# Optimization experiments

Measured on AMD Instinct MI355X. Metric: run time of the kernel, lower is better.

## Reference

```python
import jax, jax.numpy as jnp
import numpy as np

GAMMA = 5e-4
IN_DIM, HID = 512, 4096
N = HID  # batch must equal hidden_dim for classifier(gram) to type-check


def setup_inputs() -> dict:
    key = jax.random.key(0)
    ks = jax.random.split(key, 7)
    s = lambda fan_in: 1.0 / np.sqrt(fan_in)
    return {
        "x": jax.random.normal(ks[0], (N, IN_DIM), jnp.float32),
        "W1": jax.random.uniform(ks[1], (HID, IN_DIM), jnp.float32, -s(IN_DIM), s(IN_DIM)),
        "b1": jax.random.uniform(ks[2], (HID,), jnp.float32, -s(IN_DIM), s(IN_DIM)),
        "W2": jax.random.uniform(ks[3], (HID, HID), jnp.float32, -s(HID), s(HID)),
        "b2": jax.random.uniform(ks[4], (HID,), jnp.float32, -s(HID), s(HID)),
        "Wc": jax.random.uniform(ks[5], (1, HID), jnp.float32, -s(HID), s(HID)),
        "bc": jax.random.uniform(ks[6], (1,), jnp.float32, -s(HID), s(HID)),
    }


def reference(x, W1, b1, W2, b2, Wc, bc):
    h = jnp.tanh(x @ W1.T + b1)          # [N, HID]
    h = jnp.tanh(h @ W2.T + b2)          # [N, HID]
    # KernelLayer: support = h.detach() (first call), RBF gram via cdist+exp
    support = jax.lax.stop_gradient(h)   # [N, HID]
    sq = (jnp.sum(h * h, axis=1, keepdims=True)
          + jnp.sum(support * support, axis=1)[None, :]
          - 2.0 * (h @ support.T))       # [N, N] squared distances
    gram = jnp.exp(-GAMMA * sq)
    return gram @ Wc.T + bc              # [N, 1]
```

## Files before the change

### kernel.cpp

```cpp
#include <hip/hip_runtime.h>
#include <hip/hip_bf16.h>


#define NROWS 4096
#define HID   4096
#define INDIM 512
#define GAMMA_F 5e-4f

typedef float f32x4  __attribute__((ext_vector_type(4)));
typedef int   i32x4  __attribute__((ext_vector_type(4)));
typedef int   i32x8  __attribute__((ext_vector_type(8)));

#define SCALE1 0x7F7F7F7F

#define MFMA16(d, a, b) \
    d = __builtin_amdgcn_mfma_scale_f32_16x16x128_f8f6f4( \
        a, b, d, 0, 0, 0, SCALE1, 0, SCALE1)

__device__ __forceinline__ unsigned char f2e4m3(float x) {
  unsigned int u = __float_as_uint(x);
  unsigned char s = (unsigned char)((u >> 24) & 0x80u);
  float a = fabsf(x);
  if (a >= 448.f) return s | 0x7E;
  if (a < 0.015625f) {
    int q = (int)rintf(a * 512.f);
    return s | (unsigned char)q;
  }
  unsigned int ua = u & 0x7fffffffu;
  ua += 0x7FFFFu + ((ua >> 20) & 1u);
  int e = (int)(ua >> 23) - 127;
  unsigned int m = (ua >> 20) & 7u;
  return s | (unsigned char)(((e + 7) << 3) | m);
}

__global__ void prep(const float* __restrict__ x, const float* __restrict__ W1,
                     const float* __restrict__ W2, const float* __restrict__ bc,
                     unsigned char* __restrict__ xq, unsigned char* __restrict__ w1q,
                     unsigned char* __restrict__ w2q,
                     float* __restrict__ out, float* __restrict__ norms) {
  const int gi = blockIdx.x * blockDim.x + threadIdx.x;
  if (gi < NROWS) { out[gi] = bc[0]; norms[gi] = 0.f; }
  const int NX  = NROWS * INDIM / 8;
  const int NW2 = HID * HID / 8;
  const int total = 2 * NX + NW2;
  const int stride = gridDim.x * blockDim.x;
  for (int i = gi; i < total; i += stride) {
    const float* src; unsigned char* dst; float sc; int j;
    if (i < NX)          { src = x;  dst = xq;  sc = 16.f;  j = i; }
    else if (i < 2 * NX) { src = W1; dst = w1q; sc = 32.f;  j = i - NX; }
    else                 { src = W2; dst = w2q; sc = 128.f; j = i - 2 * NX; }
    float4 v0 = ((const float4*)src)[j * 2];
    float4 v1 = ((const float4*)src)[j * 2 + 1];
    unsigned int r0 = (unsigned int)f2e4m3(v0.x * sc)
                    | ((unsigned int)f2e4m3(v0.y * sc) << 8)
                    | ((unsigned int)f2e4m3(v0.z * sc) << 16)
                    | ((unsigned int)f2e4m3(v0.w * sc) << 24);
    unsigned int r1 = (unsigned int)f2e4m3(v1.x * sc)
                    | ((unsigned int)f2e4m3(v1.y * sc) << 8)
                    | ((unsigned int)f2e4m3(v1.z * sc) << 16)
                    | ((unsigned int)f2e4m3(v1.w * sc) << 24);
    uint2 o; o.x = r0; o.y = r1;
    ((uint2*)dst)[j] = o;
  }
}

__device__ __forceinline__ void gload16(const void* g, void* l) {
  __builtin_amdgcn_global_load_lds(
      (const __attribute__((address_space(1))) void*)g,
      (__attribute__((address_space(3))) void*)l, 16, 0, 0);
}

#define LDFRAG(dst, base0, off, RSTRIDE) do {                       \
    i32x4 lo_ = *(const i32x4*)((base0) + (off));                   \
    i32x4 hi_ = *(const i32x4*)((base0) + (RSTRIDE) + (off));       \
    dst = __builtin_shufflevector(lo_, hi_, 0, 1, 2, 3, 4, 5, 6, 7); } while (0)

template <int EPI>
__global__ __launch_bounds__(256, 4)
void gemm128_fp8(const unsigned char* __restrict__ A, const unsigned char* __restrict__ B,
                 int K, int N,
                 const float* __restrict__ bias, unsigned char* __restrict__ Hout,
                 float* __restrict__ norms_out) {
  __shared__ __align__(16) unsigned char As[2][128 * 64];
  __shared__ __align__(16) unsigned char Bs[2][128 * 64];

  const int tid  = threadIdx.x;
  const int lane = tid & 63;
  const int wave = tid >> 6;
  const int wr = wave >> 1, wc = wave & 1;
  const int fr = lane & 15, fq = lane >> 4;

  const int nwg = gridDim.x;
  const int cpx = nwg >> 3;
  const int bid = blockIdx.x;
  const int swzb = (bid & 7) * cpx + (bid >> 3);
  const int nbx = N >> 7;
  const int brow = (swzb / nbx) << 7;
  const int bcol = (swzb % nbx) << 7;

  const unsigned char* ap[4]; const unsigned char* bp[4]; int ldq[4];
#pragma unroll
  for (int q = 0; q < 4; ++q) {
    int idx = q * 256 + tid;
    int h   = idx >> 9;
    int row = (idx >> 2) & 127;
    int c   = idx & 3;
    int gcol = ((((c ^ ((row >> 1) & 3)) << 1) | h) << 4);
    ap[q] = A + (size_t)(brow + row) * K + gcol;
    bp[q] = B + (size_t)(bcol + row) * K + gcol;
    ldq[q] = (q * 256 + wave * 64) * 16;
  }

  int aoff[4], boff[4];
#pragma unroll
  for (int mi = 0; mi < 4; ++mi) {
    int row = wr * 64 + mi * 16 + fr;
    aoff[mi] = row * 64 + ((fq ^ ((row >> 1) & 3)) << 4);
  }
#pragma unroll
  for (int nj = 0; nj < 4; ++nj) {
    int row = wc * 64 + nj * 16 + fr;
    boff[nj] = row * 64 + ((fq ^ ((row >> 1) & 3)) << 4);
  }

  f32x4 acc[4][4] = {};

  for (int t = 0; t < (K >> 7); ++t) {
    __syncthreads();
    {
      int kk = t * 128;
      gload16(ap[0] + kk, &As[0][0] + ldq[0]);
      gload16(ap[1] + kk, &As[0][0] + ldq[1]);
      gload16(ap[2] + kk, &As[0][0] + ldq[2]);
      gload16(ap[3] + kk, &As[0][0] + ldq[3]);
      gload16(bp[0] + kk, &Bs[0][0] + ldq[0]);
      gload16(bp[1] + kk, &Bs[0][0] + ldq[1]);
      gload16(bp[2] + kk, &Bs[0][0] + ldq[2]);
      gload16(bp[3] + kk, &Bs[0][0] + ldq[3]);
    }
    __syncthreads();

    i32x8 af[4], bf[4];
#pragma unroll
    for (int mi = 0; mi < 4; ++mi) LDFRAG(af[mi], &As[0][0], aoff[mi], 8192);
#pragma unroll
    for (int nj = 0; nj < 4; ++nj) LDFRAG(bf[nj], &Bs[0][0], boff[nj], 8192);
#pragma unroll
    for (int mi = 0; mi < 4; ++mi)
#pragma unroll
      for (int nj = 0; nj < 4; ++nj) MFMA16(acc[mi][nj], af[mi], bf[nj]);
  }

  const float rescale = (EPI == 0) ? (1.f / 512.f) : (1.f / 1024.f);
  float bv[4];
#pragma unroll
  for (int nj = 0; nj < 4; ++nj) bv[nj] = bias[bcol + wc * 64 + nj * 16 + fr];
#pragma unroll
  for (int mi = 0; mi < 4; ++mi) {
    int row0 = brow + wr * 64 + mi * 16 + fq * 4;
#pragma unroll
    for (int rr = 0; rr < 4; ++rr) {
      float ns = 0.f;
#pragma unroll
      for (int nj = 0; nj < 4; ++nj) {
        int col = bcol + wc * 64 + nj * 16 + fr;
        float v = tanhf(acc[mi][nj][rr] * rescale + bv[nj]);
        Hout[(size_t)(row0 + rr) * N + col] = f2e4m3(8.f * v);
        if (EPI == 2) ns += v * v;
      }
      if (EPI == 2) {
        ns += __shfl_xor(ns, 1);
        ns += __shfl_xor(ns, 2);
        ns += __shfl_xor(ns, 4);
        ns += __shfl_xor(ns, 8);
        if (fr == 0) atomicAdd(&norms_out[row0 + rr], ns);
      }
    }
  }
}

__global__ __launch_bounds__(256, 2)
void gram_tri(const unsigned char* __restrict__ H, int K,
              const float* __restrict__ norms, const float* __restrict__ Wc,
              float* __restrict__ out) {
  __shared__ __align__(16) unsigned char As[2][128 * 64];
  __shared__ __align__(16) unsigned char Bs[2][128 * 64];

  const int tid  = threadIdx.x;
  const int lane = tid & 63;
  const int wave = tid >> 6;
  const int wr = wave >> 1, wc = wave & 1;
  const int fr = lane & 15, fq = lane >> 4;

  const int bid = blockIdx.x;
  const int swzb = (bid & 7) * 66 + (bid >> 3);
  int I = (int)((sqrtf(8.0f * (float)swzb + 1.0f) - 1.0f) * 0.5f);
  while ((I + 1) * (I + 2) / 2 <= swzb) ++I;
  while (I * (I + 1) / 2 > swzb) --I;
  const int J = swzb - I * (I + 1) / 2;
  const int brow = I << 7, bcol = J << 7;
  const bool diag = (I == J);

  const unsigned char* ap[4]; const unsigned char* bp[4]; int wq[4];
#pragma unroll
  for (int q = 0; q < 4; ++q) {
    int idx = q * 256 + tid;
    int h   = idx >> 9;
    int row = (idx >> 2) & 127;
    int c   = idx & 3;
    int gcol = ((((c ^ ((row >> 1) & 3)) << 1) | h) << 4);
    ap[q] = H + (size_t)(brow + row) * K + gcol;
    bp[q] = H + (size_t)(bcol + row) * K + gcol;
    wq[q] = idx * 16;
  }

  int aoff[4], boff[4];
#pragma unroll
  for (int mi = 0; mi < 4; ++mi) {
    int row = wr * 64 + mi * 16 + fr;
    aoff[mi] = row * 64 + ((fq ^ ((row >> 1) & 3)) << 4);
  }
#pragma unroll
  for (int nj = 0; nj < 4; ++nj) {
    int row = wc * 64 + nj * 16 + fr;
    boff[nj] = row * 64 + ((fq ^ ((row >> 1) & 3)) << 4);
  }

  const int NT = K >> 7;
  f32x4 acc[4][4] = {};
  i32x4 rA[4], rB[4];

#pragma unroll
  for (int q = 0; q < 4; ++q) {
    rA[q] = *(const i32x4*)(ap[q]);
    rB[q] = *(const i32x4*)(bp[q]);
  }
#pragma unroll
  for (int q = 0; q < 4; ++q) {
    *(i32x4*)(&As[0][0] + wq[q]) = rA[q];
    *(i32x4*)(&Bs[0][0] + wq[q]) = rB[q];
  }
  __syncthreads();

  for (int t = 0; t < NT; ++t) {
    int tn = t + 1; if (tn >= NT) tn = NT - 1;
#pragma unroll
    for (int q = 0; q < 4; ++q) {
      rA[q] = *(const i32x4*)(ap[q] + tn * 128);
      rB[q] = *(const i32x4*)(bp[q] + tn * 128);
    }

    i32x8 af[4], bf[4];
#pragma unroll
    for (int mi = 0; mi < 4; ++mi) LDFRAG(af[mi], &As[0][0], aoff[mi], 8192);
#pragma unroll
    for (int nj = 0; nj < 4; ++nj) LDFRAG(bf[nj], &Bs[0][0], boff[nj], 8192);
#pragma unroll
    for (int mi = 0; mi < 4; ++mi)
#pragma unroll
      for (int nj = 0; nj < 4; ++nj)
        acc[mi][nj] = __builtin_amdgcn_mfma_scale_f32_16x16x128_f8f6f4(
            af[mi], bf[nj], acc[mi][nj], 0, 0, 0, SCALE1, 0, SCALE1);

    __syncthreads();
#pragma unroll
    for (int q = 0; q < 4; ++q) {
      *(i32x4*)(&As[0][0] + wq[q]) = rA[q];
      *(i32x4*)(&Bs[0][0] + wq[q]) = rB[q];
    }
    __syncthreads();
  }

  float ncol[4], wcv[4];
#pragma unroll
  for (int nj = 0; nj < 4; ++nj) {
    int col = bcol + wc * 64 + nj * 16 + fr;
    ncol[nj] = norms[col];
    wcv[nj]  = Wc[col];
  }
  float colpart[4] = {0.f, 0.f, 0.f, 0.f};
#pragma unroll
  for (int mi = 0; mi < 4; ++mi) {
    int row0 = brow + wr * 64 + mi * 16 + fq * 4;
    float4 nr4  = *(const float4*)&norms[row0];
    float4 wcr4 = *(const float4*)&Wc[row0];
#pragma unroll
    for (int rr = 0; rr < 4; ++rr) {
      float nrow = (rr == 0) ? nr4.x : (rr == 1) ? nr4.y : (rr == 2) ? nr4.z : nr4.w;
      float wrow = (rr == 0) ? wcr4.x : (rr == 1) ? wcr4.y : (rr == 2) ? wcr4.z : wcr4.w;
      float rowpart = 0.f;
#pragma unroll
      for (int nj = 0; nj < 4; ++nj) {
        float sq = nrow + ncol[nj] - acc[mi][nj][rr] * 0.03125f;
        float e = __expf(-GAMMA_F * sq);
        rowpart += e * wcv[nj];
        colpart[nj] += e * wrow;
      }
      rowpart += __shfl_xor(rowpart, 1);
      rowpart += __shfl_xor(rowpart, 2);
      rowpart += __shfl_xor(rowpart, 4);
      rowpart += __shfl_xor(rowpart, 8);
      if (fr == 0) atomicAdd(&out[row0 + rr], rowpart);
    }
  }
  if (!diag) {
#pragma unroll
    for (int nj = 0; nj < 4; ++nj) {
      colpart[nj] += __shfl_xor(colpart[nj], 16);
      colpart[nj] += __shfl_xor(colpart[nj], 32);
      if (fq == 0) atomicAdd(&out[bcol + wc * 64 + nj * 16 + fr], colpart[nj]);
    }
  }
}

extern "C" void kernel_launch(void* const* d_in, const int* in_sizes, int n_in,
                              void* d_out, int out_size, void* d_ws, size_t ws_size,
                              hipStream_t stream) {
  const float* x  = (const float*)d_in[0];
  const float* W1 = (const float*)d_in[1];
  const float* b1 = (const float*)d_in[2];
  const float* W2 = (const float*)d_in[3];
  const float* b2 = (const float*)d_in[4];
  const float* Wc = (const float*)d_in[5];
  const float* bc = (const float*)d_in[6];
  float* out = (float*)d_out;

  char* ws = (char*)d_ws;
  unsigned char* xq  = (unsigned char*)ws; ws += (size_t)NROWS * INDIM;
  unsigned char* w1q = (unsigned char*)ws; ws += (size_t)HID * INDIM;
  unsigned char* w2q = (unsigned char*)ws; ws += (size_t)HID * HID;
  unsigned char* h1q = (unsigned char*)ws; ws += (size_t)NROWS * HID;
  unsigned char* h2q = (unsigned char*)ws; ws += (size_t)NROWS * HID;
  float* norms = (float*)ws;                ws += (size_t)NROWS * 4;

  prep<<<2048, 256, 0, stream>>>(x, W1, W2, bc, xq, w1q, w2q, out, norms);

  const int grid = (NROWS / 128) * (HID / 128);

  gemm128_fp8<0><<<grid, 256, 0, stream>>>(xq, w1q, INDIM, HID, b1, h1q, nullptr);
  gemm128_fp8<2><<<grid, 256, 0, stream>>>(h1q, w2q, HID, HID, b2, h2q, norms);
  gram_tri<<<528, 256, 0, stream>>>(h2q, HID, norms, Wc, out);
}
```

Baseline: 199.4 us.

## Retile symmetric gram kernel to 64x128 tiles with direct global-to-LDS loads

```diff
diff --git a/kernel.cpp b/kernel.cpp
--- a/kernel.cpp
+++ b/kernel.cpp
@@ -179,11 +179,11 @@
   }
 }
 
-__global__ __launch_bounds__(256, 2)
+__global__ __launch_bounds__(256, 4)
 void gram_tri(const unsigned char* __restrict__ H, int K,
               const float* __restrict__ norms, const float* __restrict__ Wc,
               float* __restrict__ out) {
-  __shared__ __align__(16) unsigned char As[2][128 * 64];
+  __shared__ __align__(16) unsigned char As[2][64 * 64];
   __shared__ __align__(16) unsigned char Bs[2][128 * 64];
 
   const int tid  = threadIdx.x;
@@ -193,15 +193,27 @@
   const int fr = lane & 15, fq = lane >> 4;
 
   const int bid = blockIdx.x;
-  const int swzb = (bid & 7) * 66 + (bid >> 3);
-  int I = (int)((sqrtf(8.0f * (float)swzb + 1.0f) - 1.0f) * 0.5f);
-  while ((I + 1) * (I + 2) / 2 <= swzb) ++I;
-  while (I * (I + 1) / 2 > swzb) --I;
-  const int J = swzb - I * (I + 1) / 2;
-  const int brow = I << 7, bcol = J << 7;
-  const bool diag = (I == J);
-
-  const unsigned char* ap[4]; const unsigned char* bp[4]; int wq[4];
+  const int swzb = (bid & 7) * 132 + (bid >> 3);
+  int J = (int)((65.f - sqrtf(4225.f - 4.f * (float)swzb)) * 0.5f);
+  if (J < 0) J = 0; if (J > 31) J = 31;
+  while (J < 31 && (J + 1) * (64 - J) <= swzb) ++J;
+  while (J > 0 && J * (65 - J) > swzb) --J;
+  const int I = 2 * J + (swzb - J * (65 - J));
+  const int brow = I << 6, bcol = J << 7;
+  const bool full = (I >= 2 * J + 2);
+
+  const unsigned char* ap[2]; int ldqa[2];
+#pragma unroll
+  for (int q = 0; q < 2; ++q) {
+    int idx = q * 256 + tid;
+    int h   = idx >> 8;
+    int row = (idx >> 2) & 63;
+    int c   = idx & 3;
+    int gcol = ((((c ^ ((row >> 1) & 3)) << 1) | h) << 4);
+    ap[q] = H + (size_t)(brow + row) * K + gcol;
+    ldqa[q] = (q * 256 + wave * 64) * 16;
+  }
+  const unsigned char* bp[4]; int ldqb[4];
 #pragma unroll
   for (int q = 0; q < 4; ++q) {
     int idx = q * 256 + tid;
@@ -209,15 +221,14 @@
     int row = (idx >> 2) & 127;
     int c   = idx & 3;
     int gcol = ((((c ^ ((row >> 1) & 3)) << 1) | h) << 4);
-    ap[q] = H + (size_t)(brow + row) * K + gcol;
     bp[q] = H + (size_t)(bcol + row) * K + gcol;
-    wq[q] = idx * 16;
-  }
-
-  int aoff[4], boff[4];
-#pragma unroll
-  for (int mi = 0; mi < 4; ++mi) {
-    int row = wr * 64 + mi * 16 + fr;
+    ldqb[q] = (q * 256 + wave * 64) * 16;
+  }
+
+  int aoff[2], boff[4];
+#pragma unroll
+  for (int mi = 0; mi < 2; ++mi) {
+    int row = wr * 32 + mi * 16 + fr;
     aoff[mi] = row * 64 + ((fq ^ ((row >> 1) & 3)) << 4);
   }
 #pragma unroll
@@ -226,66 +237,49 @@
     boff[nj] = row * 64 + ((fq ^ ((row >> 1) & 3)) << 4);
   }
 
-  const int NT = K >> 7;
-  f32x4 acc[4][4] = {};
-  i32x4 rA[4], rB[4];
-
-#pragma unroll
-  for (int q = 0; q < 4; ++q) {
-    rA[q] = *(const i32x4*)(ap[q]);
-    rB[q] = *(const i32x4*)(bp[q]);
-  }
-#pragma unroll
-  for (int q = 0; q < 4; ++q) {
-    *(i32x4*)(&As[0][0] + wq[q]) = rA[q];
-    *(i32x4*)(&Bs[0][0] + wq[q]) = rB[q];
-  }
-  __syncthreads();
-
-  for (int t = 0; t < NT; ++t) {
-    int tn = t + 1; if (tn >= NT) tn = NT - 1;
-#pragma unroll
-    for (int q = 0; q < 4; ++q) {
-      rA[q] = *(const i32x4*)(ap[q] + tn * 128);
-      rB[q] = *(const i32x4*)(bp[q] + tn * 128);
-    }
-
-    i32x8 af[4], bf[4];
-#pragma unroll
-    for (int mi = 0; mi < 4; ++mi) LDFRAG(af[mi], &As[0][0], aoff[mi], 8192);
-#pragma unroll
-    for (int nj = 0; nj < 4; ++nj) LDFRAG(bf[nj], &Bs[0][0], boff[nj], 8192);
-#pragma unroll
-    for (int mi = 0; mi < 4; ++mi)
-#pragma unroll
-      for (int nj = 0; nj < 4; ++nj)
-        acc[mi][nj] = __builtin_amdgcn_mfma_scale_f32_16x16x128_f8f6f4(
-            af[mi], bf[nj], acc[mi][nj], 0, 0, 0, SCALE1, 0, SCALE1);
-
+  f32x4 acc[2][4] = {};
+
+  for (int t = 0; t < (K >> 7); ++t) {
     __syncthreads();
-#pragma unroll
-    for (int q = 0; q < 4; ++q) {
-      *(i32x4*)(&As[0][0] + wq[q]) = rA[q];
-      *(i32x4*)(&Bs[0][0] + wq[q]) = rB[q];
+    {
+      int kk = t * 128;
+      gload16(ap[0] + kk, &As[0][0] + ldqa[0]);
+      gload16(ap[1] + kk, &As[0][0] + ldqa[1]);
+      gload16(bp[0] + kk, &Bs[0][0] + ldqb[0]);
+      gload16(bp[1] + kk, &Bs[0][0] + ldqb[1]);
+      gload16(bp[2] + kk, &Bs[0][0] + ldqb[2]);
+      gload16(bp[3] + kk, &Bs[0][0] + ldqb[3]);
     }
     __syncthreads();
+
+    i32x8 af[2], bf[4];
+#pragma unroll
+    for (int mi = 0; mi < 2; ++mi) LDFRAG(af[mi], &As[0][0], aoff[mi], 4096);
+#pragma unroll
+    for (int nj = 0; nj < 4; ++nj) LDFRAG(bf[nj], &Bs[0][0], boff[nj], 8192);
+#pragma unroll
+    for (int mi = 0; mi < 2; ++mi)
+#pragma unroll
+      for (int nj = 0; nj < 4; ++nj) MFMA16(acc[mi][nj], af[mi], bf[nj]);
   }
 
   float ncol[4], wcv[4];
+  int colv[4];
 #pragma unroll
   for (int nj = 0; nj < 4; ++nj) {
-    int col = bcol + wc * 64 + nj * 16 + fr;
-    ncol[nj] = norms[col];
-    wcv[nj]  = Wc[col];
+    colv[nj] = bcol + wc * 64 + nj * 16 + fr;
+    ncol[nj] = norms[colv[nj]];
+    wcv[nj]  = Wc[colv[nj]];
   }
   float colpart[4] = {0.f, 0.f, 0.f, 0.f};
 #pragma unroll
-  for (int mi = 0; mi < 4; ++mi) {
-    int row0 = brow + wr * 64 + mi * 16 + fq * 4;
+  for (int mi = 0; mi < 2; ++mi) {
+    int row0 = brow + wr * 32 + mi * 16 + fq * 4;
     float4 nr4  = *(const float4*)&norms[row0];
     float4 wcr4 = *(const float4*)&Wc[row0];
 #pragma unroll
     for (int rr = 0; rr < 4; ++rr) {
+      int r = row0 + rr;
       float nrow = (rr == 0) ? nr4.x : (rr == 1) ? nr4.y : (rr == 2) ? nr4.z : nr4.w;
       float wrow = (rr == 0) ? wcr4.x : (rr == 1) ? wcr4.y : (rr == 2) ? wcr4.z : wcr4.w;
       float rowpart = 0.f;
@@ -293,23 +287,26 @@
       for (int nj = 0; nj < 4; ++nj) {
         float sq = nrow + ncol[nj] - acc[mi][nj][rr] * 0.03125f;
         float e = __expf(-GAMMA_F * sq);
-        rowpart += e * wcv[nj];
-        colpart[nj] += e * wrow;
+        if (full) {
+          rowpart += e * wcv[nj];
+          colpart[nj] += e * wrow;
+        } else {
+          rowpart += (r >= colv[nj]) ? e * wcv[nj] : 0.f;
+          colpart[nj] += (r > colv[nj]) ? e * wrow : 0.f;
+        }
       }
       rowpart += __shfl_xor(rowpart, 1);
       rowpart += __shfl_xor(rowpart, 2);
       rowpart += __shfl_xor(rowpart, 4);
       rowpart += __shfl_xor(rowpart, 8);
-      if (fr == 0) atomicAdd(&out[row0 + rr], rowpart);
+      if (fr == 0) atomicAdd(&out[r], rowpart);
     }
   }
-  if (!diag) {
-#pragma unroll
-    for (int nj = 0; nj < 4; ++nj) {
-      colpart[nj] += __shfl_xor(colpart[nj], 16);
-      colpart[nj] += __shfl_xor(colpart[nj], 32);
-      if (fq == 0) atomicAdd(&out[bcol + wc * 64 + nj * 16 + fr], colpart[nj]);
-    }
+#pragma unroll
+  for (int nj = 0; nj < 4; ++nj) {
+    colpart[nj] += __shfl_xor(colpart[nj], 16);
+    colpart[nj] += __shfl_xor(colpart[nj], 32);
+    if (fq == 0) atomicAdd(&out[colv[nj]], colpart[nj]);
   }
 }
 
@@ -339,5 +336,5 @@
 
   gemm128_fp8<0><<<grid, 256, 0, stream>>>(xq, w1q, INDIM, HID, b1, h1q, nullptr);
   gemm128_fp8<2><<<grid, 256, 0, stream>>>(h1q, w2q, HID, HID, b2, h2q, norms);
-  gram_tri<<<528, 256, 0, stream>>>(h2q, HID, norms, Wc, out);
-}
+  gram_tri<<<1056, 256, 0, stream>>>(h2q, HID, norms, Wc, out);
+}
```

Result: slower. 207.4 us (+4.0%).

## Use direct global-to-LDS loads with doubled K-step in gram kernel

Applied to the files above, without the earlier changes.

```diff
diff --git a/kernel.cpp b/kernel.cpp
--- a/kernel.cpp
+++ b/kernel.cpp
@@ -183,8 +183,8 @@
 void gram_tri(const unsigned char* __restrict__ H, int K,
               const float* __restrict__ norms, const float* __restrict__ Wc,
               float* __restrict__ out) {
-  __shared__ __align__(16) unsigned char As[2][128 * 64];
-  __shared__ __align__(16) unsigned char Bs[2][128 * 64];
+  __shared__ __align__(16) unsigned char As[2][2][128 * 64];
+  __shared__ __align__(16) unsigned char Bs[2][2][128 * 64];
 
   const int tid  = threadIdx.x;
   const int lane = tid & 63;
@@ -201,7 +201,7 @@
   const int brow = I << 7, bcol = J << 7;
   const bool diag = (I == J);
 
-  const unsigned char* ap[4]; const unsigned char* bp[4]; int wq[4];
+  const unsigned char* ap[4]; const unsigned char* bp[4]; int ldq[4];
 #pragma unroll
   for (int q = 0; q < 4; ++q) {
     int idx = q * 256 + tid;
@@ -211,7 +211,7 @@
     int gcol = ((((c ^ ((row >> 1) & 3)) << 1) | h) << 4);
     ap[q] = H + (size_t)(brow + row) * K + gcol;
     bp[q] = H + (size_t)(bcol + row) * K + gcol;
-    wq[q] = idx * 16;
+    ldq[q] = (q * 256 + wave * 64) * 16;
   }
 
   int aoff[4], boff[4];
@@ -226,49 +226,43 @@
     boff[nj] = row * 64 + ((fq ^ ((row >> 1) & 3)) << 4);
   }
 
-  const int NT = K >> 7;
   f32x4 acc[4][4] = {};
-  i32x4 rA[4], rB[4];
-
-#pragma unroll
-  for (int q = 0; q < 4; ++q) {
-    rA[q] = *(const i32x4*)(ap[q]);
-    rB[q] = *(const i32x4*)(bp[q]);
-  }
-#pragma unroll
-  for (int q = 0; q < 4; ++q) {
-    *(i32x4*)(&As[0][0] + wq[q]) = rA[q];
-    *(i32x4*)(&Bs[0][0] + wq[q]) = rB[q];
-  }
-  __syncthreads();
-
-  for (int t = 0; t < NT; ++t) {
-    int tn = t + 1; if (tn >= NT) tn = NT - 1;
-#pragma unroll
-    for (int q = 0; q < 4; ++q) {
-      rA[q] = *(const i32x4*)(ap[q] + tn * 128);
-      rB[q] = *(const i32x4*)(bp[q] + tn * 128);
-    }
-
-    i32x8 af[4], bf[4];
-#pragma unroll
-    for (int mi = 0; mi < 4; ++mi) LDFRAG(af[mi], &As[0][0], aoff[mi], 8192);
-#pragma unroll
-    for (int nj = 0; nj < 4; ++nj) LDFRAG(bf[nj], &Bs[0][0], boff[nj], 8192);
-#pragma unroll
-    for (int mi = 0; mi < 4; ++mi)
-#pragma unroll
-      for (int nj = 0; nj < 4; ++nj)
-        acc[mi][nj] = __builtin_amdgcn_mfma_scale_f32_16x16x128_f8f6f4(
-            af[mi], bf[nj], acc[mi][nj], 0, 0, 0, SCALE1, 0, SCALE1);
-
+
+  for (int t = 0; t < (K >> 8); ++t) {
     __syncthreads();
-#pragma unroll
-    for (int q = 0; q < 4; ++q) {
-      *(i32x4*)(&As[0][0] + wq[q]) = rA[q];
-      *(i32x4*)(&Bs[0][0] + wq[q]) = rB[q];
+    {
+      int kk = t * 256;
+      gload16(ap[0] + kk, &As[0][0][0] + ldq[0]);
+      gload16(ap[1] + kk, &As[0][0][0] + ldq[1]);
+      gload16(ap[2] + kk, &As[0][0][0] + ldq[2]);
+      gload16(ap[3] + kk, &As[0][0][0] + ldq[3]);
+      gload16(bp[0] + kk, &Bs[0][0][0] + ldq[0]);
+      gload16(bp[1] + kk, &Bs[0][0][0] + ldq[1]);
+      gload16(bp[2] + kk, &Bs[0][0][0] + ldq[2]);
+      gload16(bp[3] + kk, &Bs[0][0][0] + ldq[3]);
+      gload16(ap[0] + kk + 128, &As[1][0][0] + ldq[0]);
+      gload16(ap[1] + kk + 128, &As[1][0][0] + ldq[1]);
+      gload16(ap[2] + kk + 128, &As[1][0][0] + ldq[2]);
+      gload16(ap[3] + kk + 128, &As[1][0][0] + ldq[3]);
+      gload16(bp[0] + kk + 128, &Bs[1][0][0] + ldq[0]);
+      gload16(bp[1] + kk + 128, &Bs[1][0][0] + ldq[1]);
+      gload16(bp[2] + kk + 128, &Bs[1][0][0] + ldq[2]);
+      gload16(bp[3] + kk + 128, &Bs[1][0][0] + ldq[3]);
     }
     __syncthreads();
+
+#pragma unroll
+    for (int s = 0; s < 2; ++s) {
+      i32x8 af[4], bf[4];
+#pragma unroll
+      for (int mi = 0; mi < 4; ++mi) LDFRAG(af[mi], &As[s][0][0], aoff[mi], 8192);
+#pragma unroll
+      for (int nj = 0; nj < 4; ++nj) LDFRAG(bf[nj], &Bs[s][0][0], boff[nj], 8192);
+#pragma unroll
+      for (int mi = 0; mi < 4; ++mi)
+#pragma unroll
+        for (int nj = 0; nj < 4; ++nj) MFMA16(acc[mi][nj], af[mi], bf[nj]);
+    }
   }
 
   float ncol[4], wcv[4];
```

Result: slower. 208.4 us (+4.5%).
